# Kernel tuning notes

Measured on AMD Instinct MI355X. Metric: run time of the kernel, lower is better.

## Reference

```python
import jax, jax.numpy as jnp
import numpy as np


def setup_inputs() -> dict:
    key = jax.random.key(0)
    k1, k2, k3 = jax.random.split(key, 3)
    B, T, D = 32, 512, 256
    x = jax.random.normal(k1, (B, T, D), dtype=jnp.float32)
    duration = jax.random.randint(k2, (B, T), 0, 8, dtype=jnp.int32)
    src_lens = jax.random.randint(k3, (B,), 0, 512, dtype=jnp.int32)
    max_len = 4096
    return {"x": x, "duration": duration, "src_lens": src_lens, "max_len": max_len}


def reference(x, duration, src_lens, max_len):
    # x: [B, T, D]; duration: [B, T] int; src_lens: [B] int; max_len: python int
    B, T, D = x.shape
    pos = jnp.arange(T, dtype=jnp.int32)
    # durations beyond src_len are treated as 0 (i >= frame_len branch)
    dur = jnp.where(pos[None, :] < src_lens[:, None], duration, 0)
    cum = jnp.cumsum(dur, axis=1)                     # [B, T] cumulative end frame
    tgt_len = cum[:, -1].astype(jnp.int32)            # [B] total expanded length
    frames = jnp.arange(max_len, dtype=jnp.int32)     # [L]
    # frame j belongs to the first phoneme i with cum[i] > j  (searchsorted right)
    idx = jax.vmap(lambda c: jnp.searchsorted(c, frames, side="right"))(cum)  # [B, L]
    idx = jnp.clip(idx, 0, T - 1)
    out = jnp.take_along_axis(x, idx[:, :, None], axis=1)  # [B, L, D]
    valid = frames[None, :] < tgt_len[:, None]              # [B, L]
    out = jnp.where(valid[:, :, None], out, jnp.zeros((), dtype=x.dtype))
    return out, tgt_len
```

## Files before the change

kernel.cpp:

```cpp
#include <hip/hip_runtime.h>
#include <hip/hip_bf16.h>


#define BB 32
#define TT 512
#define DD 256
#define LL 4096
#define D4 (DD / 4)
#define FPB 64
#define BPB (LL / FPB)

__global__ __launch_bounds__(256) void length_regulator_kernel(
    const float4* __restrict__ x,
    const int*    __restrict__ duration,
    const int*    __restrict__ src_lens,
    float*        __restrict__ out_f)
{
    __shared__ int sc[2][TT];

    const int b     = blockIdx.x / BPB;
    const int chunk = blockIdx.x % BPB;
    const int tid   = threadIdx.x;

    const int slen = src_lens[b];

    for (int i = tid; i < TT; i += 256) {
        int d = duration[b * TT + i];
        sc[0][i] = (i < slen) ? d : 0;
    }
    __syncthreads();

    int src = 0;
    for (int off = 1; off < TT; off <<= 1) {
        for (int i = tid; i < TT; i += 256) {
            int v = sc[src][i];
            if (i >= off) v += sc[src][i - off];
            sc[src ^ 1][i] = v;
        }
        __syncthreads();
        src ^= 1;
    }
    const int* cum = sc[src];
    const int tlen = cum[TT - 1];

    if (chunk == 0 && tid == 0) {
        out_f[(size_t)BB * LL * DD + b] = (float)tlen;
    }

    float4* out4 = (float4*)out_f;
    const int wave = tid >> 6;
    const int lane = tid & 63;

    for (int f = wave; f < FPB; f += 4) {
        const int j = chunk * FPB + f;
        float4 v;
        if (j >= tlen) {
            v = make_float4(0.f, 0.f, 0.f, 0.f);
        } else {
            int lo = 0, hi = TT;
            while (lo < hi) {
                int mid = (lo + hi) >> 1;
                if (cum[mid] > j) hi = mid; else lo = mid + 1;
            }
            int idx = lo < (TT - 1) ? lo : (TT - 1);
            v = x[((size_t)b * TT + idx) * D4 + lane];
        }
        out4[((size_t)b * LL + j) * D4 + lane] = v;
    }
}

extern "C" void kernel_launch(void* const* d_in, const int* in_sizes, int n_in,
                              void* d_out, int out_size, void* d_ws, size_t ws_size,
                              hipStream_t stream) {
    const float4* x        = (const float4*)d_in[0];
    const int*    duration = (const int*)d_in[1];
    const int*    src_lens = (const int*)d_in[2];
    float*        out_f    = (float*)d_out;

    dim3 grid(BB * BPB);
    dim3 block(256);
    length_regulator_kernel<<<grid, block, 0, stream>>>(x, duration, src_lens, out_f);
}
```

Measured before the change: 162.1 us.

## Split scan into separate kernel and early-exit zero chunks in expand

```diff
diff --git a/kernel.cpp b/kernel.cpp
--- a/kernel.cpp
+++ b/kernel.cpp
@@ -10,24 +10,20 @@
 #define FPB 64
 #define BPB (LL / FPB)
 
-__global__ __launch_bounds__(256) void length_regulator_kernel(
-    const float4* __restrict__ x,
-    const int*    __restrict__ duration,
-    const int*    __restrict__ src_lens,
-    float*        __restrict__ out_f)
+__global__ __launch_bounds__(256) void lr_scan_kernel(
+    const int* __restrict__ duration,
+    const int* __restrict__ src_lens,
+    int*       __restrict__ ws_cum,
+    int*       __restrict__ ws_tlen,
+    float*     __restrict__ out_f)
 {
     __shared__ int sc[2][TT];
-
-    const int b     = blockIdx.x / BPB;
-    const int chunk = blockIdx.x % BPB;
-    const int tid   = threadIdx.x;
-
+    const int b   = blockIdx.x;
+    const int tid = threadIdx.x;
     const int slen = src_lens[b];
 
-    for (int i = tid; i < TT; i += 256) {
-        int d = duration[b * TT + i];
-        sc[0][i] = (i < slen) ? d : 0;
-    }
+    for (int i = tid; i < TT; i += 256)
+        sc[0][i] = (i < slen) ? duration[b * TT + i] : 0;
     __syncthreads();
 
     int src = 0;
@@ -40,32 +36,65 @@
         __syncthreads();
         src ^= 1;
     }
-    const int* cum = sc[src];
-    const int tlen = cum[TT - 1];
 
-    if (chunk == 0 && tid == 0) {
+    for (int i = tid; i < TT; i += 256)
+        ws_cum[b * TT + i] = sc[src][i];
+    if (tid == 0) {
+        const int tlen = sc[src][TT - 1];
+        ws_tlen[b] = tlen;
         out_f[(size_t)BB * LL * DD + b] = (float)tlen;
     }
+}
 
-    float4* out4 = (float4*)out_f;
-    const int wave = tid >> 6;
-    const int lane = tid & 63;
+__global__ __launch_bounds__(256) void lr_expand_kernel(
+    const float4* __restrict__ x,
+    const int*    __restrict__ ws_cum,
+    const int*    __restrict__ ws_tlen,
+    float4*       __restrict__ out4)
+{
+    const int b     = blockIdx.x / BPB;
+    const int chunk = blockIdx.x % BPB;
+    const int tid   = threadIdx.x;
+    const int lane  = tid & 63;
+    const int wave  = tid >> 6;
+    const int j0    = chunk * FPB;
+    const int tlen  = ws_tlen[b];
+    const float4 zero = make_float4(0.f, 0.f, 0.f, 0.f);
 
-    for (int f = wave; f < FPB; f += 4) {
-        const int j = chunk * FPB + f;
-        float4 v;
-        if (j >= tlen) {
-            v = make_float4(0.f, 0.f, 0.f, 0.f);
-        } else {
+    if (j0 >= tlen) {
+        #pragma unroll 4
+        for (int f = wave; f < FPB; f += 4)
+            out4[((size_t)b * LL + j0 + f) * D4 + lane] = zero;
+        return;
+    }
+
+    __shared__ int cum[TT];
+    __shared__ int idxs[FPB];
+
+    for (int i = tid; i < TT; i += 256)
+        cum[i] = ws_cum[b * TT + i];
+    __syncthreads();
+
+    if (tid < FPB) {
+        const int j = j0 + tid;
+        int idx = -1;
+        if (j < tlen) {
             int lo = 0, hi = TT;
             while (lo < hi) {
-                int mid = (lo + hi) >> 1;
+                const int mid = (lo + hi) >> 1;
                 if (cum[mid] > j) hi = mid; else lo = mid + 1;
             }
-            int idx = lo < (TT - 1) ? lo : (TT - 1);
-            v = x[((size_t)b * TT + idx) * D4 + lane];
+            idx = lo < (TT - 1) ? lo : (TT - 1);
         }
-        out4[((size_t)b * LL + j) * D4 + lane] = v;
+        idxs[tid] = idx;
+    }
+    __syncthreads();
+
+    #pragma unroll 4
+    for (int f = wave; f < FPB; f += 4) {
+        const int idx = idxs[f];
+        const float4 v = (idx >= 0) ? x[((size_t)b * TT + idx) * D4 + lane] : zero;
+        out4[((size_t)b * LL + j0 + f) * D4 + lane] = v;
     }
 }
 
@@ -77,7 +106,9 @@
     const int*    src_lens = (const int*)d_in[2];
     float*        out_f    = (float*)d_out;
 
-    dim3 grid(BB * BPB);
-    dim3 block(256);
-    length_regulator_kernel<<<grid, block, 0, stream>>>(x, duration, src_lens, out_f);
+    int* ws_cum  = (int*)d_ws;
+    int* ws_tlen = ws_cum + BB * TT;
+
+    lr_scan_kernel<<<dim3(BB), dim3(256), 0, stream>>>(duration, src_lens, ws_cum, ws_tlen, out_f);
+    lr_expand_kernel<<<dim3(BB * BPB), dim3(256), 0, stream>>>(x, ws_cum, ws_tlen, (float4*)out_f);
 }
```

Measured after the change: 164.5 us. No clear change (+1.5%).
